# Kernel tuning notes

Hardware: AMD Instinct MI355X
Metric: run time of the kernel (lower is better)

Reference implementation:

```python
import jax, jax.numpy as jnp
import numpy as np

N, K, D = 8192, 128, 512

def setup_inputs() -> dict:
    key = jax.random.key(0)
    kx, kc = jax.random.split(key)
    x = jax.random.normal(kx, (N, D), dtype=jnp.float32)
    centroids = jax.random.normal(kc, (K, D), dtype=jnp.float32)
    return {"x": x, "centroids": centroids}

def reference(x, centroids):
    # Faithful to torch: dist = (x[:,None,:] - centroids[None]).norm(2, dim=2)
    # Broadcast subtract -> [N, K, D] intermediate, then L2 reduction over D.
    diff = x[:, None, :] - centroids[None, :, :]          # [N, K, D]
    dist = jnp.sqrt(jnp.sum(diff * diff, axis=2))         # [N, K]
    return dist
```

## Files before the change

kernel.cpp:

```cpp
#include <hip/hip_runtime.h>
#include <hip/hip_bf16.h>

#define N_ROWS 8192
#define K_CENT 128
#define D_DIM  512

typedef short v8s __attribute__((ext_vector_type(8)));
typedef float v4f __attribute__((ext_vector_type(4)));

__device__ inline unsigned short f2bf(float f) {
    union { float f; unsigned u; } v; v.f = f;
    unsigned r = v.u + 0x7FFFu + ((v.u >> 16) & 1u);
    return (unsigned short)(r >> 16);
}

__global__ __launch_bounds__(256) void prep_centroids(const float* __restrict__ c,
                                                      float* __restrict__ cnorm,
                                                      unsigned short* __restrict__ cb) {
    int wave = (int)((blockIdx.x * blockDim.x + threadIdx.x) >> 6);
    int lane = threadIdx.x & 63;
    if (wave >= K_CENT) return;
    const float* src = c + (size_t)wave * D_DIM;
    float4 a = ((const float4*)src)[lane];
    float4 b = ((const float4*)src)[64 + lane];
    float s = a.x*a.x + a.y*a.y + a.z*a.z + a.w*a.w
            + b.x*b.x + b.y*b.y + b.z*b.z + b.w*b.w;
    #pragma unroll
    for (int off = 32; off >= 1; off >>= 1) s += __shfl_xor(s, off, 64);
    if (lane == 0) cnorm[wave] = s;
    unsigned short* dst = cb + (size_t)wave * D_DIM;
    ushort4 p0, p1;
    p0.x = f2bf(a.x); p0.y = f2bf(a.y); p0.z = f2bf(a.z); p0.w = f2bf(a.w);
    p1.x = f2bf(b.x); p1.y = f2bf(b.y); p1.z = f2bf(b.z); p1.w = f2bf(b.w);
    ((ushort4*)dst)[lane]      = p0;
    ((ushort4*)dst)[64 + lane] = p1;
}

__global__ __launch_bounds__(64) void dist_kernel(const float* __restrict__ x,
                                                  const unsigned short* __restrict__ cb,
                                                  const float* __restrict__ cnorm,
                                                  float* __restrict__ out) {
    const int lane = threadIdx.x;
    const int n16  = lane & 15;
    const int quad = lane >> 4;
    const int rowbase = blockIdx.x * 16;

    const float* xptr = x + (size_t)(rowbase + n16) * D_DIM + quad * 8;
    const unsigned short* bptr = cb + (size_t)n16 * D_DIM + quad * 8;

    v4f acc[8];
    #pragma unroll
    for (int g = 0; g < 8; ++g) acc[g] = (v4f){0.f, 0.f, 0.f, 0.f};

    float sn = 0.f;

    for (int kk = 0; kk < D_DIM; kk += 32) {
        float4 a0 = *(const float4*)(xptr);
        float4 a1 = *(const float4*)(xptr + 4);
        sn += a0.x*a0.x + a0.y*a0.y + a0.z*a0.z + a0.w*a0.w
            + a1.x*a1.x + a1.y*a1.y + a1.z*a1.z + a1.w*a1.w;
        v8s afrag;
        afrag[0] = (short)f2bf(a0.x); afrag[1] = (short)f2bf(a0.y);
        afrag[2] = (short)f2bf(a0.z); afrag[3] = (short)f2bf(a0.w);
        afrag[4] = (short)f2bf(a1.x); afrag[5] = (short)f2bf(a1.y);
        afrag[6] = (short)f2bf(a1.z); afrag[7] = (short)f2bf(a1.w);
        #pragma unroll
        for (int g = 0; g < 8; ++g) {
            v8s bfrag = *(const v8s*)(bptr + (size_t)g * 16 * D_DIM);
            acc[g] = __builtin_amdgcn_mfma_f32_16x16x32_bf16(afrag, bfrag, acc[g], 0, 0, 0);
        }
        xptr += 32;
        bptr += 32;
    }

    sn += __shfl_xor(sn, 16, 64);
    sn += __shfl_xor(sn, 32, 64);

    float xn[4];
    #pragma unroll
    for (int r = 0; r < 4; ++r) xn[r] = __shfl(sn, quad * 4 + r, 64);

    #pragma unroll
    for (int g = 0; g < 8; ++g) {
        float cn = cnorm[g * 16 + n16];
        #pragma unroll
        for (int r = 0; r < 4; ++r) {
            float d2 = xn[r] + cn - 2.0f * acc[g][r];
            d2 = d2 > 0.f ? d2 : 0.f;
            out[(size_t)(rowbase + quad * 4 + r) * K_CENT + g * 16 + n16] = sqrtf(d2);
        }
    }
}

__global__ void naive_kernel(const float* __restrict__ x, const float* __restrict__ c,
                             float* __restrict__ out) {
    int idx = blockIdx.x * blockDim.x + threadIdx.x;
    if (idx >= N_ROWS * K_CENT) return;
    int n = idx / K_CENT, k = idx % K_CENT;
    const float* xr = x + (size_t)n * D_DIM;
    const float* cr = c + (size_t)k * D_DIM;
    float s = 0.f;
    for (int d = 0; d < D_DIM; ++d) { float df = xr[d] - cr[d]; s += df * df; }
    out[idx] = sqrtf(s);
}

extern "C" void kernel_launch(void* const* d_in, const int* in_sizes, int n_in,
                              void* d_out, int out_size, void* d_ws, size_t ws_size,
                              hipStream_t stream) {
    const float* x = (const float*)d_in[0];
    const float* c = (const float*)d_in[1];
    float* out = (float*)d_out;

    const size_t need = 512 + (size_t)K_CENT * D_DIM * sizeof(unsigned short);
    if (ws_size < need) {
        int total = N_ROWS * K_CENT;
        naive_kernel<<<(total + 255) / 256, 256, 0, stream>>>(x, c, out);
        return;
    }

    float* cnorm = (float*)d_ws;
    unsigned short* cb = (unsigned short*)((char*)d_ws + 512);

    prep_centroids<<<(K_CENT * 64 + 255) / 256, 256, 0, stream>>>(c, cnorm, cb);
    dist_kernel<<<N_ROWS / 16, 64, 0, stream>>>(x, cb, cnorm, out);
}
```

Baseline: 76.73 us.

## Split centroid groups across four waves per block with preloaded A fragments

The distance kernel now launches 256-thread blocks in which each of four waves handles two of the eight 16-centroid groups for the same 16 rows. Each wave first loads and converts its whole x tile into 16 bf16 fragments, then runs a fully unrolled MFMA loop over two accumulators. This raises the number of waves in flight and shortens each wave's dependent MFMA chain, to hide memory latency. The cost is that every wave redundantly loads and converts the x rows and uses more registers for the preloaded fragments.

```diff
diff --git a/kernel.cpp b/kernel.cpp
--- a/kernel.cpp
+++ b/kernel.cpp
@@ -36,56 +36,61 @@
     ((ushort4*)dst)[64 + lane] = p1;
 }
 
-__global__ __launch_bounds__(64) void dist_kernel(const float* __restrict__ x,
-                                                  const unsigned short* __restrict__ cb,
-                                                  const float* __restrict__ cnorm,
-                                                  float* __restrict__ out) {
-    const int lane = threadIdx.x;
+__global__ __launch_bounds__(256) void dist_kernel(const float* __restrict__ x,
+                                                   const unsigned short* __restrict__ cb,
+                                                   const float* __restrict__ cnorm,
+                                                   float* __restrict__ out) {
+    const int lane = threadIdx.x & 63;
+    const int wave = threadIdx.x >> 6;
     const int n16  = lane & 15;
     const int quad = lane >> 4;
     const int rowbase = blockIdx.x * 16;
+    const int g0 = wave * 2;
 
     const float* xptr = x + (size_t)(rowbase + n16) * D_DIM + quad * 8;
-    const unsigned short* bptr = cb + (size_t)n16 * D_DIM + quad * 8;
-
-    v4f acc[8];
+    v8s afrag[16];
+    float sn = 0.f;
     #pragma unroll
-    for (int g = 0; g < 8; ++g) acc[g] = (v4f){0.f, 0.f, 0.f, 0.f};
-
-    float sn = 0.f;
-
-    for (int kk = 0; kk < D_DIM; kk += 32) {
-        float4 a0 = *(const float4*)(xptr);
-        float4 a1 = *(const float4*)(xptr + 4);
+    for (int i = 0; i < 16; ++i) {
+        float4 a0 = *(const float4*)(xptr + i * 32);
+        float4 a1 = *(const float4*)(xptr + i * 32 + 4);
         sn += a0.x*a0.x + a0.y*a0.y + a0.z*a0.z + a0.w*a0.w
             + a1.x*a1.x + a1.y*a1.y + a1.z*a1.z + a1.w*a1.w;
-        v8s afrag;
-        afrag[0] = (short)f2bf(a0.x); afrag[1] = (short)f2bf(a0.y);
-        afrag[2] = (short)f2bf(a0.z); afrag[3] = (short)f2bf(a0.w);
-        afrag[4] = (short)f2bf(a1.x); afrag[5] = (short)f2bf(a1.y);
-        afrag[6] = (short)f2bf(a1.z); afrag[7] = (short)f2bf(a1.w);
-        #pragma unroll
-        for (int g = 0; g < 8; ++g) {
-            v8s bfrag = *(const v8s*)(bptr + (size_t)g * 16 * D_DIM);
-            acc[g] = __builtin_amdgcn_mfma_f32_16x16x32_bf16(afrag, bfrag, acc[g], 0, 0, 0);
-        }
-        xptr += 32;
-        bptr += 32;
+        v8s f;
+        f[0] = (short)f2bf(a0.x); f[1] = (short)f2bf(a0.y);
+        f[2] = (short)f2bf(a0.z); f[3] = (short)f2bf(a0.w);
+        f[4] = (short)f2bf(a1.x); f[5] = (short)f2bf(a1.y);
+        f[6] = (short)f2bf(a1.z); f[7] = (short)f2bf(a1.w);
+        afrag[i] = f;
+    }
+
+    const unsigned short* b0 = cb + (size_t)(g0 * 16 + n16) * D_DIM + quad * 8;
+    const unsigned short* b1 = b0 + (size_t)16 * D_DIM;
+
+    v4f acc0 = (v4f){0.f, 0.f, 0.f, 0.f};
+    v4f acc1 = (v4f){0.f, 0.f, 0.f, 0.f};
+    #pragma unroll
+    for (int i = 0; i < 16; ++i) {
+        v8s bf0 = *(const v8s*)(b0 + i * 32);
+        v8s bf1 = *(const v8s*)(b1 + i * 32);
+        acc0 = __builtin_amdgcn_mfma_f32_16x16x32_bf16(afrag[i], bf0, acc0, 0, 0, 0);
+        acc1 = __builtin_amdgcn_mfma_f32_16x16x32_bf16(afrag[i], bf1, acc1, 0, 0, 0);
     }
 
     sn += __shfl_xor(sn, 16, 64);
     sn += __shfl_xor(sn, 32, 64);
-
     float xn[4];
     #pragma unroll
     for (int r = 0; r < 4; ++r) xn[r] = __shfl(sn, quad * 4 + r, 64);
 
     #pragma unroll
-    for (int g = 0; g < 8; ++g) {
+    for (int gi = 0; gi < 2; ++gi) {
+        int g = g0 + gi;
         float cn = cnorm[g * 16 + n16];
+        v4f acc = gi ? acc1 : acc0;
         #pragma unroll
         for (int r = 0; r < 4; ++r) {
-            float d2 = xn[r] + cn - 2.0f * acc[g][r];
+            float d2 = xn[r] + cn - 2.0f * acc[r];
             d2 = d2 > 0.f ? d2 : 0.f;
             out[(size_t)(rowbase + quad * 4 + r) * K_CENT + g * 16 + n16] = sqrtf(d2);
         }
@@ -122,5 +127,5 @@
     unsigned short* cb = (unsigned short*)((char*)d_ws + 512);
 
     prep_centroids<<<(K_CENT * 64 + 255) / 256, 256, 0, stream>>>(c, cnorm, cb);
-    dist_kernel<<<N_ROWS / 16, 64, 0, stream>>>(x, cb, cnorm, out);
+    dist_kernel<<<N_ROWS / 16, 256, 0, stream>>>(x, cb, cnorm, out);
 }
```

Measured after the change: 78.19 us. Within noise of the previous version (+1.9%).

## Pre-convert x to bf16 in prep pass and split centroid groups across waves

Applied to the files above, without the earlier changes.

The prep kernel now converts every x row to bf16 and computes the row norms, along with the centroids. The distance kernel reads bf16 fragments directly and spreads the 8 centroid groups over 4 waves per block and 2 blocks per row tile, so each wave owns one accumulator. This removes the per-tile fp32 conversion work and raises the number of waves in flight. In exchange it adds a write and re-read of an 8 MB bf16 copy of x, and each x tile is now read by 8 waves instead of 1.

```diff
diff --git a/kernel.cpp b/kernel.cpp
--- a/kernel.cpp
+++ b/kernel.cpp
@@ -14,21 +14,38 @@
     return (unsigned short)(r >> 16);
 }
 
-__global__ __launch_bounds__(256) void prep_centroids(const float* __restrict__ c,
-                                                      float* __restrict__ cnorm,
-                                                      unsigned short* __restrict__ cb) {
+__global__ __launch_bounds__(256) void prep_all(const float* __restrict__ x,
+                                                const float* __restrict__ c,
+                                                unsigned short* __restrict__ xb,
+                                                unsigned short* __restrict__ cb,
+                                                float* __restrict__ xnorm,
+                                                float* __restrict__ cnorm) {
     int wave = (int)((blockIdx.x * blockDim.x + threadIdx.x) >> 6);
     int lane = threadIdx.x & 63;
-    if (wave >= K_CENT) return;
-    const float* src = c + (size_t)wave * D_DIM;
+    if (wave >= N_ROWS + K_CENT) return;
+
+    const float* src;
+    unsigned short* dst;
+    float* nrm;
+    if (wave < N_ROWS) {
+        src = x + (size_t)wave * D_DIM;
+        dst = xb + (size_t)wave * D_DIM;
+        nrm = xnorm + wave;
+    } else {
+        int r = wave - N_ROWS;
+        src = c + (size_t)r * D_DIM;
+        dst = cb + (size_t)r * D_DIM;
+        nrm = cnorm + r;
+    }
+
     float4 a = ((const float4*)src)[lane];
     float4 b = ((const float4*)src)[64 + lane];
     float s = a.x*a.x + a.y*a.y + a.z*a.z + a.w*a.w
             + b.x*b.x + b.y*b.y + b.z*b.z + b.w*b.w;
     #pragma unroll
     for (int off = 32; off >= 1; off >>= 1) s += __shfl_xor(s, off, 64);
-    if (lane == 0) cnorm[wave] = s;
-    unsigned short* dst = cb + (size_t)wave * D_DIM;
+    if (lane == 0) *nrm = s;
+
     ushort4 p0, p1;
     p0.x = f2bf(a.x); p0.y = f2bf(a.y); p0.z = f2bf(a.z); p0.w = f2bf(a.w);
     p1.x = f2bf(b.x); p1.y = f2bf(b.y); p1.z = f2bf(b.z); p1.w = f2bf(b.w);
@@ -36,59 +53,39 @@
     ((ushort4*)dst)[64 + lane] = p1;
 }
 
-__global__ __launch_bounds__(64) void dist_kernel(const float* __restrict__ x,
-                                                  const unsigned short* __restrict__ cb,
-                                                  const float* __restrict__ cnorm,
-                                                  float* __restrict__ out) {
-    const int lane = threadIdx.x;
+__global__ __launch_bounds__(256, 3) void dist_kernel(const unsigned short* __restrict__ xb,
+                                                      const unsigned short* __restrict__ cb,
+                                                      const float* __restrict__ xnorm,
+                                                      const float* __restrict__ cnorm,
+                                                      float* __restrict__ out) {
+    const int lane = threadIdx.x & 63;
+    const int wave = threadIdx.x >> 6;
     const int n16  = lane & 15;
     const int quad = lane >> 4;
-    const int rowbase = blockIdx.x * 16;
 
-    const float* xptr = x + (size_t)(rowbase + n16) * D_DIM + quad * 8;
-    const unsigned short* bptr = cb + (size_t)n16 * D_DIM + quad * 8;
+    const int tile = blockIdx.x >> 1;
+    const int half = blockIdx.x & 1;
+    const int rowbase = tile * 16;
+    const int g = half * 4 + wave;
 
-    v4f acc[8];
+    const unsigned short* aptr = xb + (size_t)(rowbase + n16) * D_DIM + quad * 8;
+    const unsigned short* bptr = cb + (size_t)(g * 16 + n16) * D_DIM + quad * 8;
+
+    v4f acc = (v4f){0.f, 0.f, 0.f, 0.f};
     #pragma unroll
-    for (int g = 0; g < 8; ++g) acc[g] = (v4f){0.f, 0.f, 0.f, 0.f};
-
-    float sn = 0.f;
-
-    for (int kk = 0; kk < D_DIM; kk += 32) {
-        float4 a0 = *(const float4*)(xptr);
-        float4 a1 = *(const float4*)(xptr + 4);
-        sn += a0.x*a0.x + a0.y*a0.y + a0.z*a0.z + a0.w*a0.w
-            + a1.x*a1.x + a1.y*a1.y + a1.z*a1.z + a1.w*a1.w;
-        v8s afrag;
-        afrag[0] = (short)f2bf(a0.x); afrag[1] = (short)f2bf(a0.y);
-        afrag[2] = (short)f2bf(a0.z); afrag[3] = (short)f2bf(a0.w);
-        afrag[4] = (short)f2bf(a1.x); afrag[5] = (short)f2bf(a1.y);
-        afrag[6] = (short)f2bf(a1.z); afrag[7] = (short)f2bf(a1.w);
-        #pragma unroll
-        for (int g = 0; g < 8; ++g) {
-            v8s bfrag = *(const v8s*)(bptr + (size_t)g * 16 * D_DIM);
-            acc[g] = __builtin_amdgcn_mfma_f32_16x16x32_bf16(afrag, bfrag, acc[g], 0, 0, 0);
-        }
-        xptr += 32;
-        bptr += 32;
+    for (int i = 0; i < 16; ++i) {
+        v8s af = *(const v8s*)(aptr + i * 32);
+        v8s bf = *(const v8s*)(bptr + i * 32);
+        acc = __builtin_amdgcn_mfma_f32_16x16x32_bf16(af, bf, acc, 0, 0, 0);
     }
 
-    sn += __shfl_xor(sn, 16, 64);
-    sn += __shfl_xor(sn, 32, 64);
-
-    float xn[4];
+    const float cn = cnorm[g * 16 + n16];
     #pragma unroll
-    for (int r = 0; r < 4; ++r) xn[r] = __shfl(sn, quad * 4 + r, 64);
-
-    #pragma unroll
-    for (int g = 0; g < 8; ++g) {
-        float cn = cnorm[g * 16 + n16];
-        #pragma unroll
-        for (int r = 0; r < 4; ++r) {
-            float d2 = xn[r] + cn - 2.0f * acc[g][r];
-            d2 = d2 > 0.f ? d2 : 0.f;
-            out[(size_t)(rowbase + quad * 4 + r) * K_CENT + g * 16 + n16] = sqrtf(d2);
-        }
+    for (int r = 0; r < 4; ++r) {
+        int row = rowbase + quad * 4 + r;
+        float d2 = xnorm[row] + cn - 2.0f * acc[r];
+        d2 = d2 > 0.f ? d2 : 0.f;
+        out[(size_t)row * K_CENT + g * 16 + n16] = sqrtf(d2);
     }
 }
 
@@ -111,16 +108,24 @@
     const float* c = (const float*)d_in[1];
     float* out = (float*)d_out;
 
-    const size_t need = 512 + (size_t)K_CENT * D_DIM * sizeof(unsigned short);
+    const size_t xb_off = 0;
+    const size_t cb_off = (size_t)N_ROWS * D_DIM * sizeof(unsigned short);
+    const size_t xn_off = cb_off + (size_t)K_CENT * D_DIM * sizeof(unsigned short);
+    const size_t cn_off = xn_off + (size_t)N_ROWS * sizeof(float);
+    const size_t need   = cn_off + (size_t)K_CENT * sizeof(float);
+
     if (ws_size < need) {
         int total = N_ROWS * K_CENT;
         naive_kernel<<<(total + 255) / 256, 256, 0, stream>>>(x, c, out);
         return;
     }
 
-    float* cnorm = (float*)d_ws;
-    unsigned short* cb = (unsigned short*)((char*)d_ws + 512);
+    unsigned short* xb = (unsigned short*)((char*)d_ws + xb_off);
+    unsigned short* cb = (unsigned short*)((char*)d_ws + cb_off);
+    float* xnorm = (float*)((char*)d_ws + xn_off);
+    float* cnorm = (float*)((char*)d_ws + cn_off);
 
-    prep_centroids<<<(K_CENT * 64 + 255) / 256, 256, 0, stream>>>(c, cnorm, cb);
-    dist_kernel<<<N_ROWS / 16, 64, 0, stream>>>(x, cb, cnorm, out);
+    const int total_rows = N_ROWS + K_CENT;
+    prep_all<<<(total_rows * 64 + 255) / 256, 256, 0, stream>>>(x, c, xb, cb, xnorm, cnorm);
+    dist_kernel<<<(N_ROWS / 16) * 2, 256, 0, stream>>>(xb, cb, xnorm, cnorm, out);
 }
```

New measurement: 82.61 us. 1.08x slower.

## Stage x tile in LDS as bf16 and split centroid groups across waves

Applied to the files above, without the earlier changes.

Each block now converts a 16-row x tile to bf16 once into padded LDS. Four waves each compute one 16-centroid group, and the grid is doubled so each block covers half of the centroids. This replaces the single-wave-per-block design, which had low occupancy and serial MFMA chains. The row norms now come from the diagonal of an x·xᵀ MFMA instead of scalar FMAs, so they use bf16-rounded x, which may loosen accuracy. The x tile is read from global memory twice, once per half.

```diff
diff --git a/kernel.cpp b/kernel.cpp
--- a/kernel.cpp
+++ b/kernel.cpp
@@ -4,6 +4,7 @@
 #define N_ROWS 8192
 #define K_CENT 128
 #define D_DIM  512
+#define LDS_PITCH 520
 
 typedef short v8s __attribute__((ext_vector_type(8)));
 typedef float v4f __attribute__((ext_vector_type(4)));
@@ -36,59 +37,56 @@
     ((ushort4*)dst)[64 + lane] = p1;
 }
 
-__global__ __launch_bounds__(64) void dist_kernel(const float* __restrict__ x,
-                                                  const unsigned short* __restrict__ cb,
-                                                  const float* __restrict__ cnorm,
-                                                  float* __restrict__ out) {
-    const int lane = threadIdx.x;
+__global__ __launch_bounds__(256, 4) void dist_kernel(const float* __restrict__ x,
+                                                      const unsigned short* __restrict__ cb,
+                                                      const float* __restrict__ cnorm,
+                                                      float* __restrict__ out) {
+    __shared__ unsigned short xlds[16 * LDS_PITCH];
+
+    const int t    = threadIdx.x;
+    const int lane = t & 63;
+    const int wave = t >> 6;
+    const int half = blockIdx.x >> 9;
+    const int tile = blockIdx.x & 511;
+    const int rowbase = tile * 16;
+    const int g = half * 4 + wave;
+
+    const float* xs = x + (size_t)rowbase * D_DIM;
+    #pragma unroll
+    for (int j = 0; j < 8; ++j) {
+        int f = (j * 256 + t) * 4;
+        float4 v = *(const float4*)(xs + f);
+        int row = f >> 9;
+        int k   = f & 511;
+        ushort4 p;
+        p.x = f2bf(v.x); p.y = f2bf(v.y); p.z = f2bf(v.z); p.w = f2bf(v.w);
+        *(ushort4*)&xlds[row * LDS_PITCH + k] = p;
+    }
+    __syncthreads();
+
     const int n16  = lane & 15;
     const int quad = lane >> 4;
-    const int rowbase = blockIdx.x * 16;
+    const unsigned short* bptr = cb + (size_t)(g * 16 + n16) * D_DIM + quad * 8;
+    const unsigned short* aptr = &xlds[n16 * LDS_PITCH + quad * 8];
 
-    const float* xptr = x + (size_t)(rowbase + n16) * D_DIM + quad * 8;
-    const unsigned short* bptr = cb + (size_t)n16 * D_DIM + quad * 8;
-
-    v4f acc[8];
+    v4f acc  = (v4f){0.f, 0.f, 0.f, 0.f};
+    v4f accx = (v4f){0.f, 0.f, 0.f, 0.f};
     #pragma unroll
-    for (int g = 0; g < 8; ++g) acc[g] = (v4f){0.f, 0.f, 0.f, 0.f};
-
-    float sn = 0.f;
-
-    for (int kk = 0; kk < D_DIM; kk += 32) {
-        float4 a0 = *(const float4*)(xptr);
-        float4 a1 = *(const float4*)(xptr + 4);
-        sn += a0.x*a0.x + a0.y*a0.y + a0.z*a0.z + a0.w*a0.w
-            + a1.x*a1.x + a1.y*a1.y + a1.z*a1.z + a1.w*a1.w;
-        v8s afrag;
-        afrag[0] = (short)f2bf(a0.x); afrag[1] = (short)f2bf(a0.y);
-        afrag[2] = (short)f2bf(a0.z); afrag[3] = (short)f2bf(a0.w);
-        afrag[4] = (short)f2bf(a1.x); afrag[5] = (short)f2bf(a1.y);
-        afrag[6] = (short)f2bf(a1.z); afrag[7] = (short)f2bf(a1.w);
-        #pragma unroll
-        for (int g = 0; g < 8; ++g) {
-            v8s bfrag = *(const v8s*)(bptr + (size_t)g * 16 * D_DIM);
-            acc[g] = __builtin_amdgcn_mfma_f32_16x16x32_bf16(afrag, bfrag, acc[g], 0, 0, 0);
-        }
-        xptr += 32;
-        bptr += 32;
+    for (int i = 0; i < 16; ++i) {
+        v8s af = *(const v8s*)(aptr + i * 32);
+        v8s bf = *(const v8s*)(bptr + i * 32);
+        acc  = __builtin_amdgcn_mfma_f32_16x16x32_bf16(af, bf, acc, 0, 0, 0);
+        accx = __builtin_amdgcn_mfma_f32_16x16x32_bf16(af, af, accx, 0, 0, 0);
     }
 
-    sn += __shfl_xor(sn, 16, 64);
-    sn += __shfl_xor(sn, 32, 64);
-
-    float xn[4];
+    const float cn = cnorm[g * 16 + n16];
     #pragma unroll
-    for (int r = 0; r < 4; ++r) xn[r] = __shfl(sn, quad * 4 + r, 64);
-
-    #pragma unroll
-    for (int g = 0; g < 8; ++g) {
-        float cn = cnorm[g * 16 + n16];
-        #pragma unroll
-        for (int r = 0; r < 4; ++r) {
-            float d2 = xn[r] + cn - 2.0f * acc[g][r];
-            d2 = d2 > 0.f ? d2 : 0.f;
-            out[(size_t)(rowbase + quad * 4 + r) * K_CENT + g * 16 + n16] = sqrtf(d2);
-        }
+    for (int r = 0; r < 4; ++r) {
+        float xn = __shfl(accx[r], 20 * quad + r, 64);
+        int row = rowbase + quad * 4 + r;
+        float d2 = xn + cn - 2.0f * acc[r];
+        d2 = d2 > 0.f ? d2 : 0.f;
+        out[(size_t)row * K_CENT + g * 16 + n16] = sqrtf(d2);
     }
 }
 
@@ -122,5 +120,5 @@
     unsigned short* cb = (unsigned short*)((char*)d_ws + 512);
 
     prep_centroids<<<(K_CENT * 64 + 255) / 256, 256, 0, stream>>>(c, cnorm, cb);
-    dist_kernel<<<N_ROWS / 16, 64, 0, stream>>>(x, cb, cnorm, out);
+    dist_kernel<<<(N_ROWS / 16) * 2, 256, 0, stream>>>(x, cb, cnorm, out);
 }
```

New measurement: 74.28 us. 3.2% less time.
